# Kernel optimization log

Measured on AMD Instinct MI355X. Metric: run time of the kernel, lower is better.

Reference implementation:

```python
import jax, jax.numpy as jnp
import numpy as np

B, G, T, N = 2, 4, 64, 300
D = 256          # detr_dim == feature_dim
R = 4            # ffn_dim_ratio
MD = 32          # motion_dim


def _xavier(key, shape):
    lim = (6.0 / (shape[0] + shape[1])) ** 0.5
    return jax.random.uniform(key, shape, jnp.float32, -lim, lim)


def setup_inputs() -> dict:
    key = jax.random.key(0)
    ks = jax.random.split(key, 16)
    feats = jax.random.normal(ks[0], (B, G, T, N, D), jnp.float32)
    boxes = jax.random.uniform(ks[1], (B, G, T, N, 4), jnp.float32)
    masks = jax.random.bernoulli(ks[2], 0.3, (B, G, T, N))
    # per-trajectory permutation of frame ids 0..T-1 (unique -> unambiguous scatter)
    u = jax.random.uniform(ks[3], (B, G, N, T))
    times = jnp.swapaxes(jnp.argsort(u, axis=-1).astype(jnp.int32), 2, 3)  # [B,G,T,N]
    return {
        'trajectory_features': feats,
        'trajectory_boxes': boxes,
        'trajectory_masks': masks,
        'trajectory_times': times,
        'adp_w1': _xavier(ks[4], (D, D * R)), 'adp_b1': jnp.zeros((D * R,), jnp.float32),
        'adp_w2': _xavier(ks[5], (D * R, D)), 'adp_b2': jnp.zeros((D,), jnp.float32),
        'norm_g': jnp.ones((D,), jnp.float32), 'norm_b': jnp.zeros((D,), jnp.float32),
        'mot_w1': _xavier(ks[6], (12, MD // 2)), 'mot_b1': jnp.zeros((MD // 2,), jnp.float32),
        'mot_w2': _xavier(ks[7], (MD // 2, MD)), 'mot_b2': jnp.zeros((MD,), jnp.float32),
        'fus_w1': _xavier(ks[8], (D + MD, D)), 'fus_b1': jnp.zeros((D,), jnp.float32),
        'fus_w2': _xavier(ks[9], (D, D)), 'fus_b2': jnp.zeros((D,), jnp.float32),
        'ffn_w1': _xavier(ks[10], (D, D * R)), 'ffn_b1': jnp.zeros((D * R,), jnp.float32),
        'ffn_w2': _xavier(ks[11], (D * R, D)), 'ffn_b2': jnp.zeros((D,), jnp.float32),
        'fnorm_g': jnp.ones((D,), jnp.float32), 'fnorm_b': jnp.zeros((D,), jnp.float32),
    }


def _ffn(x, w1, b1, w2, b2):
    return jax.nn.gelu(x @ w1 + b1, approximate=False) @ w2 + b2


def _ln(x, g, b):
    m = x.mean(-1, keepdims=True)
    v = ((x - m) ** 2).mean(-1, keepdims=True)
    return (x - m) / jnp.sqrt(v + 1e-5) * g + b


def _motion_features(boxes, masks, times, mot_w1, mot_b1, mot_w2, mot_b2):
    # boxes [B,G,T,N,4] -> trajectory-major [B,G,N,T,*]
    b_, g_, t_, n_ = masks.shape
    md = mot_b2.shape[0]
    bx = jnp.swapaxes(boxes, 2, 3)              # [B,G,N,T,4]
    valid = ~jnp.swapaxes(masks, 2, 3)          # [B,G,N,T]
    tm = jnp.swapaxes(times, 2, 3)              # [B,G,N,T]
    # sort valid entries first, by time (stable)
    order = jnp.argsort(jnp.where(valid, tm, t_ + 1), axis=-1)
    sb = jnp.take_along_axis(bx, order[..., None], axis=3)   # sorted boxes
    st = jnp.take_along_axis(tm, order, axis=-1)             # sorted times
    cnt = valid.sum(-1)                                      # [B,G,N]
    pos = jnp.arange(t_)
    in_count = pos[None, None, None, :] < cnt[..., None]
    dt = jnp.maximum(st - jnp.roll(st, 1, axis=-1), 1).astype(sb.dtype)[..., None]
    mask_v = ((pos >= 1)[None, None, None, :] & in_count)[..., None]
    vel = jnp.where(mask_v, (sb - jnp.roll(sb, 1, axis=3)) / dt, 0.0)
    mask_a = ((pos >= 2)[None, None, None, :] & in_count)[..., None]
    acc = jnp.where(mask_a, (vel - jnp.roll(vel, 1, axis=3)) / dt, 0.0)
    mv = jnp.concatenate([sb, vel, acc], axis=-1)            # [B,G,N,T,12]
    enc = jax.nn.gelu(mv @ mot_w1 + mot_b1, approximate=False) @ mot_w2 + mot_b2
    write = in_count & (cnt >= 2)[..., None] & (st < t_)
    frame = jnp.where(write, st, t_)                         # t_ -> dropped
    bi, gi, ni, ti = jnp.meshgrid(jnp.arange(b_), jnp.arange(g_), jnp.arange(n_),
                                  jnp.arange(t_), indexing='ij')
    out = jnp.zeros((b_, g_, t_, n_, md), sb.dtype)
    return out.at[bi, gi, frame, ni].set(enc, mode='drop')


def reference(trajectory_features, trajectory_boxes, trajectory_masks, trajectory_times,
              adp_w1, adp_b1, adp_w2, adp_b2, norm_g, norm_b,
              mot_w1, mot_b1, mot_w2, mot_b2,
              fus_w1, fus_b1, fus_w2, fus_b2,
              ffn_w1, ffn_b1, ffn_w2, ffn_b2, fnorm_g, fnorm_b):
    x = trajectory_features + _ffn(trajectory_features, adp_w1, adp_b1, adp_w2, adp_b2)
    x = _ln(x, norm_g, norm_b)
    motion = _motion_features(trajectory_boxes, trajectory_masks, trajectory_times,
                              mot_w1, mot_b1, mot_w2, mot_b2)
    cat = jnp.concatenate([x, motion], axis=-1)
    fused = jax.nn.gelu(cat @ fus_w1 + fus_b1, approximate=False) @ fus_w2 + fus_b2
    fused = fused + _ffn(fused, ffn_w1, ffn_b1, ffn_w2, ffn_b2)
    fused = _ln(fused, fnorm_g, fnorm_b)
    return fused, motion
```

## Files before the change

### kernel.cpp

```cpp
#include <hip/hip_runtime.h>

typedef __bf16 bf16x8 __attribute__((ext_vector_type(8)));
typedef __bf16 bf16x4 __attribute__((ext_vector_type(4)));
typedef float f32x4 __attribute__((ext_vector_type(4)));

namespace {

constexpr int T_ = 64;
constexpr int N_ = 300;
constexpr int MD_ = 32;
constexpr int BG_ = 8;
constexpr long MROWS_ = (long)BG_ * T_ * N_;
constexpr long FUSED_N = MROWS_ * 256;
constexpr int MB = 32;

constexpr long PA1 = 0;
constexpr long PA2 = 262144;
constexpr long PF1 = 524288;
constexpr long PF2 = 598016;
constexpr long PN1 = 663552;
constexpr long PN2 = 925696;

__device__ __forceinline__ float gelu_f(float x) {
  const float x2 = x * x;
  const float z2 = x * fmaf(x2, 0.07135481627f, 1.5957691216f);
  const float t = __builtin_amdgcn_rcpf(1.0f + __expf(z2));
  return x * (1.0f - t);
}

__device__ __forceinline__ float gelu_exact(float x) {
  return 0.5f * x * (1.0f + erff(x * 0.7071067811865476f));
}

__global__ void k_zero_flag(int* f) { *f = 0; }

__global__ void k_detect_mask(const unsigned char* __restrict__ m, int nbytes,
                              int* __restrict__ f) {
  int i = blockIdx.x * 256 + threadIdx.x;
  if (i < nbytes && (i & 3) != 0 && m[i] != 0) atomicOr(f, 1);
}

__global__ __launch_bounds__(256)
void k_motion(const float* __restrict__ boxes, const void* __restrict__ masks,
              const int* __restrict__ times,
              const float* __restrict__ mw1, const float* __restrict__ mb1,
              const float* __restrict__ mw2, const float* __restrict__ mb2,
              float* __restrict__ motion, const int* __restrict__ flagp) {
  __shared__ int slot[4][T_];
  __shared__ int sts[4][T_];
  __shared__ float sbx[4][T_][4];
  __shared__ float otile[4][T_][MD_];
  const int tid = threadIdx.x;
  const int w = tid >> 6, l = tid & 63;
  const int traj = blockIdx.x * 4 + w;
  const int bg = traj / N_, n = traj - bg * N_;
  const int isbool = *flagp;
  const long idx = ((long)bg * T_ + l) * N_ + n;
  const bool msk = isbool ? (((const unsigned char*)masks)[idx] != 0)
                          : (((const int*)masks)[idx] != 0);
  const bool valid = !msk;
  const int tm = times[idx];

  slot[w][l] = -1;
  sts[w][l] = 0;
  *(float4*)&sbx[w][l][0] = make_float4(0.f, 0.f, 0.f, 0.f);
  __syncthreads();
  if (valid) slot[w][tm] = l;
  __syncthreads();

  const int ot = slot[w][l];
  const bool vp = ot >= 0;
  const unsigned long long bal = __ballot(vp);
  const int cnt = __builtin_popcountll(bal);
  const int pos = __builtin_popcountll(bal & ((1ull << l) - 1ull));
  if (vp) {
    sts[w][pos] = l;
    const float4 bx = *(const float4*)(boxes + (((long)bg * T_ + ot) * N_ + n) * 4);
    *(float4*)&sbx[w][pos][0] = bx;
  }
  __syncthreads();

  const int stp = sts[w][l];
  const int stm1 = sts[w][(l + 63) & 63];
  const float4 sb = *(const float4*)&sbx[w][l][0];
  const float4 sbm = *(const float4*)&sbx[w][(l + 63) & 63][0];
  const float dt = (float)max(stp - stm1, 1);
  const float inv = 1.0f / dt;
  const bool okv = (l >= 1) && (l < cnt);
  float v0 = okv ? (sb.x - sbm.x) * inv : 0.f;
  float v1 = okv ? (sb.y - sbm.y) * inv : 0.f;
  float v2 = okv ? (sb.z - sbm.z) * inv : 0.f;
  float v3 = okv ? (sb.w - sbm.w) * inv : 0.f;
  const float p0 = __shfl_up(v0, 1, 64);
  const float p1 = __shfl_up(v1, 1, 64);
  const float p2 = __shfl_up(v2, 1, 64);
  const float p3 = __shfl_up(v3, 1, 64);
  const bool oka = (l >= 2) && (l < cnt);
  const float a0 = oka ? (v0 - p0) * inv : 0.f;
  const float a1 = oka ? (v1 - p1) * inv : 0.f;
  const float a2 = oka ? (v2 - p2) * inv : 0.f;
  const float a3 = oka ? (v3 - p3) * inv : 0.f;

  const float mv[12] = {sb.x, sb.y, sb.z, sb.w, v0, v1, v2, v3, a0, a1, a2, a3};
  float e1[16];
#pragma unroll
  for (int i = 0; i < 16; ++i) {
    float a = mb1[i];
#pragma unroll
    for (int c = 0; c < 12; ++c) a = fmaf(mv[c], mw1[c * 16 + i], a);
    e1[i] = gelu_exact(a);
  }
  float enc[32];
#pragma unroll
  for (int o = 0; o < 32; ++o) {
    float a = mb2[o];
#pragma unroll
    for (int i = 0; i < 16; ++i) a = fmaf(e1[i], mw2[i * 32 + o], a);
    enc[o] = a;
  }

#pragma unroll
  for (int c = 0; c < 32; c += 4)
    *(float4*)&otile[w][l][c] = make_float4(0.f, 0.f, 0.f, 0.f);
  __syncthreads();
  if (l < cnt && cnt >= 2) {
#pragma unroll
    for (int c = 0; c < 32; ++c) otile[w][stp][c] = enc[c];
  }
  __syncthreads();

  float* mbase = motion + ((long)bg * T_ * N_ + n) * MD_;
  const float4* srcv = (const float4*)&otile[w][l][0];
  float4* dstv = (float4*)(mbase + (long)l * N_ * MD_);
#pragma unroll
  for (int q = 0; q < 8; ++q) dstv[q] = srcv[q];
}

__global__ void k_pack(const float* __restrict__ W, __bf16* __restrict__ P,
                       int K, int NN) {
  int gid = blockIdx.x * 256 + threadIdx.x;
  int total = (K >> 5) * (NN >> 4) * 64;
  if (gid >= total) return;
  int l = gid & 63, f = gid >> 6;
  int NT = NN >> 4;
  int kb = f / NT, nt = f - kb * NT;
  int krow = kb * 32 + (l >> 4) * 8;
  int col = nt * 16 + (l & 15);
  bf16x8 v;
#pragma unroll
  for (int e = 0; e < 8; ++e) v[e] = (__bf16)W[(long)(krow + e) * NN + col];
  *(bf16x8*)(P + (long)gid * 8) = v;
}

template <int NKB, bool MOT, int NT>
__device__ __forceinline__ void produce_chunk(
    const char* regA, const char* regM, char* hb, const __bf16* pb1,
    const float* b1, int r, int wid, int l, int lr, int lk) {
  const int nt0 = r * 8 + wid * 2;
  f32x4 t[2][2];
#pragma unroll
  for (int n = 0; n < 2; ++n) {
    const float4 bv = *(const float4*)(b1 + (nt0 + n) * 16 + lk * 4);
    t[n][0] = f32x4{bv.x, bv.y, bv.z, bv.w};
    t[n][1] = t[n][0];
  }
  const __bf16* wp0 = pb1 + ((long)nt0 << 9) + (l << 3);
  const __bf16* wp1 = wp0 + (1 << 9);
  bf16x8 wa0 = *(const bf16x8*)(wp0);
  bf16x8 wa1 = *(const bf16x8*)(wp1);
  bf16x8 wb0 = wa0, wb1 = wa1;
  if (NKB > 1) {
    wb0 = *(const bf16x8*)(wp0 + ((long)NT << 9));
    wb1 = *(const bf16x8*)(wp1 + ((long)NT << 9));
  }
#pragma unroll
  for (int kb = 0; kb < NKB; ++kb) {
    const bf16x8 wf0 = (kb & 1) ? wb0 : wa0;
    const bf16x8 wf1 = (kb & 1) ? wb1 : wa1;
    if (kb + 2 < NKB) {
      const bf16x8 v0 = *(const bf16x8*)(wp0 + ((long)((kb + 2) * NT) << 9));
      const bf16x8 v1 = *(const bf16x8*)(wp1 + ((long)((kb + 2) * NT) << 9));
      if (kb & 1) { wb0 = v0; wb1 = v1; } else { wa0 = v0; wa1 = v1; }
    }
    __builtin_amdgcn_s_setprio(1);
#pragma unroll
    for (int rt = 0; rt < 2; ++rt) {
      const int row = rt * 16 + lr;
      bf16x8 xf;
      if (MOT && kb == NKB - 1)
        xf = *(const bf16x8*)(regM + row * 64 + ((lk ^ (row & 3)) << 4));
      else
        xf = *(const bf16x8*)(regA + row * 512 +
                              ((((kb << 2) + lk) ^ (row & 7)) << 4));
      t[0][rt] = __builtin_amdgcn_mfma_f32_16x16x32_bf16(wf0, xf, t[0][rt], 0, 0, 0);
      t[1][rt] = __builtin_amdgcn_mfma_f32_16x16x32_bf16(wf1, xf, t[1][rt], 0, 0, 0);
    }
    __builtin_amdgcn_s_setprio(0);
  }
#pragma unroll
  for (int n = 0; n < 2; ++n)
#pragma unroll
    for (int rt = 0; rt < 2; ++rt) {
      const int row = rt * 16 + lr;
      bf16x4 hv;
#pragma unroll
      for (int e = 0; e < 4; ++e) hv[e] = (__bf16)gelu_f(t[n][rt][e]);
      *(bf16x4*)(hb + row * 256 +
                 ((wid * 64 + n * 32 + lk * 8) ^ ((row & 7) << 4))) = hv;
    }
}

__device__ __forceinline__ void consume_chunk(const char* hb,
                                              const __bf16* pb2, int kbg0,
                                              int l, int lr, int lk, int wn,
                                              f32x4 (&acc)[2][4]) {
  const __bf16* wp = pb2 + ((long)(kbg0 * 16 + wn * 4) << 9) + (l << 3);
  bf16x8 bw0[4], bw1[4];
#pragma unroll
  for (int j = 0; j < 4; ++j) bw0[j] = *(const bf16x8*)(wp + ((long)j << 9));
#pragma unroll
  for (int kbl = 0; kbl < 4; ++kbl) {
    if (kbl < 3) {
#pragma unroll
      for (int j = 0; j < 4; ++j)
        bw1[j] = *(const bf16x8*)(wp + ((long)((kbl + 1) * 16 + j) << 9));
    }
    bf16x8 a[2];
#pragma unroll
    for (int m = 0; m < 2; ++m) {
      const int row = m * 16 + lr;
      a[m] = *(const bf16x8*)(hb + row * 256 +
                              ((kbl * 64 + lk * 16) ^ ((row & 7) << 4)));
    }
    __builtin_amdgcn_s_setprio(1);
#pragma unroll
    for (int j = 0; j < 4; ++j)
#pragma unroll
      for (int m = 0; m < 2; ++m)
        acc[m][j] = __builtin_amdgcn_mfma_f32_16x16x32_bf16(a[m], bw0[j],
                                                            acc[m][j], 0, 0, 0);
    __builtin_amdgcn_s_setprio(0);
#pragma unroll
    for (int j = 0; j < 4; ++j) bw0[j] = bw1[j];
  }
}

__global__ __launch_bounds__(256, 3)
void k_mfma(const float* __restrict__ feats, const float* __restrict__ motion,
            const __bf16* __restrict__ pw,
            const float* __restrict__ ba1, const float* __restrict__ ba2,
            const float* __restrict__ ng, const float* __restrict__ nb,
            const float* __restrict__ bf1, const float* __restrict__ bf2,
            const float* __restrict__ bn1, const float* __restrict__ bn2,
            const float* __restrict__ fg, const float* __restrict__ fb,
            float* __restrict__ out) {
  __shared__ __align__(16) char smem[35840];
  char* regA = smem;
  char* hb0 = smem + 16384;
  char* hb1 = smem + 24576;
  char* regM = smem + 32768;
  float* redp = (float*)(smem + 34816);

  const int tid = threadIdx.x;
  const int l = tid & 63, wid = tid >> 6;
  const int lr = l & 15, lk = l >> 4;
  const int wn = wid;
  const int colb = wn * 64;
  const long rowbase = (long)blockIdx.x * MB;

  const __bf16* pa1 = pw + PA1;
  const __bf16* pa2 = pw + PA2;
  const __bf16* pf1 = pw + PF1;
  const __bf16* pf2 = pw + PF2;
  const __bf16* pn1 = pw + PN1;
  const __bf16* pn2 = pw + PN2;

  auto ln_stats = [&](const f32x4 (&acc)[2][4], float (&mean)[2][4],
                      float (&rstd)[2][4]) {
    float s1[2][4], s2[2][4];
#pragma unroll
    for (int m = 0; m < 2; ++m)
#pragma unroll
      for (int e = 0; e < 4; ++e) { s1[m][e] = 0.f; s2[m][e] = 0.f; }
#pragma unroll
    for (int m = 0; m < 2; ++m)
#pragma unroll
      for (int j = 0; j < 4; ++j)
#pragma unroll
        for (int e = 0; e < 4; ++e) {
          s1[m][e] += acc[m][j][e];
          s2[m][e] += acc[m][j][e] * acc[m][j][e];
        }
#pragma unroll
    for (int o = 1; o < 16; o <<= 1)
#pragma unroll
      for (int m = 0; m < 2; ++m)
#pragma unroll
        for (int e = 0; e < 4; ++e) {
          s1[m][e] += __shfl_xor(s1[m][e], o);
          s2[m][e] += __shfl_xor(s2[m][e], o);
        }
    if (lr == 0) {
#pragma unroll
      for (int m = 0; m < 2; ++m)
#pragma unroll
        for (int e = 0; e < 4; ++e) {
          const int row = m * 16 + lk * 4 + e;
          redp[(row * 4 + wn) * 2 + 0] = s1[m][e];
          redp[(row * 4 + wn) * 2 + 1] = s2[m][e];
        }
    }
    __syncthreads();
#pragma unroll
    for (int m = 0; m < 2; ++m)
#pragma unroll
      for (int e = 0; e < 4; ++e) {
        const int row = m * 16 + lk * 4 + e;
        const float S1 = redp[(row * 4 + 0) * 2] + redp[(row * 4 + 1) * 2] +
                         redp[(row * 4 + 2) * 2] + redp[(row * 4 + 3) * 2];
        const float S2 = redp[(row * 4 + 0) * 2 + 1] + redp[(row * 4 + 1) * 2 + 1] +
                         redp[(row * 4 + 2) * 2 + 1] + redp[(row * 4 + 3) * 2 + 1];
        const float mu = S1 * (1.0f / 256.0f);
        const float var = S2 * (1.0f / 256.0f) - mu * mu;
        mean[m][e] = mu;
        rstd[m][e] = rsqrtf(var + 1e-5f);
      }
  };

  f32x4 acc2[2][4];
#pragma unroll
  for (int j = 0; j < 4; ++j) {
    const int col = colb + j * 16 + lr;
    const float bv = ba2[col];
#pragma unroll
    for (int m = 0; m < 2; ++m)
#pragma unroll
      for (int e = 0; e < 4; ++e) {
        const int row = m * 16 + lk * 4 + e;
        acc2[m][j][e] = bv + feats[(rowbase + row) * 256 + col];
      }
  }
#pragma unroll
  for (int it = 0; it < 4; ++it) {
    const int c = tid + it * 256;
    const int row = c >> 5, cc = c & 31;
    const float* src = feats + (rowbase + row) * 256 + cc * 8;
    bf16x8 v;
#pragma unroll
    for (int e = 0; e < 8; ++e) v[e] = (__bf16)src[e];
    *(bf16x8*)(regA + row * 512 + ((cc ^ (row & 7)) << 4)) = v;
  }
  __syncthreads();

  produce_chunk<8, false, 64>(regA, regM, hb0, pa1, ba1, 0, wid, l, lr, lk);
  __syncthreads();
#pragma unroll 1
  for (int r = 0; r < 8; ++r) {
    if (r < 7)
      produce_chunk<8, false, 64>(regA, regM, ((r + 1) & 1) ? hb1 : hb0, pa1,
                                  ba1, r + 1, wid, l, lr, lk);
    consume_chunk((r & 1) ? hb1 : hb0, pa2, r * 4, l, lr, lk, wn, acc2);
    __syncthreads();
  }

  {
    float mean[2][4], rstd[2][4];
    ln_stats(acc2, mean, rstd);
#pragma unroll
    for (int j = 0; j < 4; ++j) {
      const int col = colb + j * 16 + lr;
      const float gv = ng[col], bv = nb[col];
#pragma unroll
      for (int m = 0; m < 2; ++m)
#pragma unroll
        for (int e = 0; e < 4; ++e) {
          const int row = m * 16 + lk * 4 + e;
          const float v = (acc2[m][j][e] - mean[m][e]) * rstd[m][e] * gv + bv;
          *(__bf16*)(regA + row * 512 + (((col >> 3) ^ (row & 7)) << 4) +
                     ((col & 7) << 1)) = (__bf16)v;
        }
    }
    if (tid < 128) {
      const int row = tid >> 2, cc = tid & 3;
      const float* src = motion + (rowbase + row) * 32 + cc * 8;
      bf16x8 v;
#pragma unroll
      for (int e = 0; e < 8; ++e) v[e] = (__bf16)src[e];
      *(bf16x8*)(regM + row * 64 + ((cc ^ (row & 3)) << 4)) = v;
    }
  }
  __syncthreads();

  {
#pragma unroll
    for (int j = 0; j < 4; ++j) {
      const float bv = bf2[colb + j * 16 + lr];
#pragma unroll
      for (int m = 0; m < 2; ++m) acc2[m][j] = {bv, bv, bv, bv};
    }
    produce_chunk<9, true, 16>(regA, regM, hb0, pf1, bf1, 0, wid, l, lr, lk);
    __syncthreads();
    produce_chunk<9, true, 16>(regA, regM, hb1, pf1, bf1, 1, wid, l, lr, lk);
    consume_chunk(hb0, pf2, 0, l, lr, lk, wn, acc2);
    __syncthreads();
    consume_chunk(hb1, pf2, 4, l, lr, lk, wn, acc2);
    __syncthreads();
#pragma unroll
    for (int j = 0; j < 4; ++j) {
      const int col = colb + j * 16 + lr;
      const float bv = bn2[col];
#pragma unroll
      for (int m = 0; m < 2; ++m)
#pragma unroll
        for (int e = 0; e < 4; ++e) {
          const int row = m * 16 + lk * 4 + e;
          const float fv = acc2[m][j][e];
          *(__bf16*)(regA + row * 512 + (((col >> 3) ^ (row & 7)) << 4) +
                     ((col & 7) << 1)) = (__bf16)fv;
          acc2[m][j][e] = fv + bv;
        }
    }
  }
  __syncthreads();

  produce_chunk<8, false, 64>(regA, regM, hb0, pn1, bn1, 0, wid, l, lr, lk);
  __syncthreads();
#pragma unroll 1
  for (int r = 0; r < 8; ++r) {
    if (r < 7)
      produce_chunk<8, false, 64>(regA, regM, ((r + 1) & 1) ? hb1 : hb0, pn1,
                                  bn1, r + 1, wid, l, lr, lk);
    consume_chunk((r & 1) ? hb1 : hb0, pn2, r * 4, l, lr, lk, wn, acc2);
    __syncthreads();
  }

  {
    float mean[2][4], rstd[2][4];
    ln_stats(acc2, mean, rstd);
#pragma unroll
    for (int j = 0; j < 4; ++j) {
      const int col = colb + j * 16 + lr;
      const float gv = fg[col], bv = fb[col];
#pragma unroll
      for (int m = 0; m < 2; ++m)
#pragma unroll
        for (int e = 0; e < 4; ++e) {
          const int row = m * 16 + lk * 4 + e;
          out[(rowbase + row) * 256 + col] =
              (acc2[m][j][e] - mean[m][e]) * rstd[m][e] * gv + bv;
        }
    }
  }
}

}

extern "C" void kernel_launch(void* const* d_in, const int* in_sizes, int n_in,
                              void* d_out, int out_size, void* d_ws, size_t ws_size,
                              hipStream_t stream) {
  const float* feats = (const float*)d_in[0];
  const float* boxes = (const float*)d_in[1];
  const void*  masks = d_in[2];
  const int*   times = (const int*)d_in[3];
  const float* wa1 = (const float*)d_in[4];
  const float* ba1 = (const float*)d_in[5];
  const float* wa2 = (const float*)d_in[6];
  const float* ba2 = (const float*)d_in[7];
  const float* ng  = (const float*)d_in[8];
  const float* nb  = (const float*)d_in[9];
  const float* mw1 = (const float*)d_in[10];
  const float* mb1 = (const float*)d_in[11];
  const float* mw2 = (const float*)d_in[12];
  const float* mb2 = (const float*)d_in[13];
  const float* wf1 = (const float*)d_in[14];
  const float* bf1 = (const float*)d_in[15];
  const float* wf2 = (const float*)d_in[16];
  const float* bf2 = (const float*)d_in[17];
  const float* wn1 = (const float*)d_in[18];
  const float* bn1 = (const float*)d_in[19];
  const float* wn2 = (const float*)d_in[20];
  const float* bn2 = (const float*)d_in[21];
  const float* fg  = (const float*)d_in[22];
  const float* fb  = (const float*)d_in[23];

  float* out_fused = (float*)d_out;
  float* out_motion = out_fused + FUSED_N;
  int* flag = (int*)d_ws;
  __bf16* pwp = (__bf16*)((char*)d_ws + 256);

  const int mask_elems = in_sizes[2];

  k_zero_flag<<<1, 1, 0, stream>>>(flag);
  k_detect_mask<<<(mask_elems + 255) / 256, 256, 0, stream>>>(
      (const unsigned char*)masks, mask_elems, flag);
  k_motion<<<(BG_ * N_) / 4, 256, 0, stream>>>(boxes, masks, times, mw1, mb1, mw2,
                                               mb2, out_motion, flag);

  auto packn = [&](const float* W, long off, int K, int NN) {
    const int total = (K / 32) * (NN / 16) * 64;
    k_pack<<<(total + 255) / 256, 256, 0, stream>>>(W, pwp + off, K, NN);
  };
  packn(wa1, PA1, 256, 1024);
  packn(wa2, PA2, 1024, 256);
  packn(wf1, PF1, 288, 256);
  packn(wf2, PF2, 256, 256);
  packn(wn1, PN1, 256, 1024);
  packn(wn2, PN2, 1024, 256);

  k_mfma<<<(int)(MROWS_ / MB), 256, 0, stream>>>(
      feats, out_motion, pwp, ba1, ba2, ng, nb, bf1, bf2, bn1, bn2, fg, fb,
      out_fused);
}
```

Baseline: 561.9 us.

## Interleave FFN up-projection and down-projection MFMAs within each pipelined round

Adds a fused_round function that runs the next chunk's first-layer MFMAs, loaded with GELU into the write buffer, in the same instruction stream as the current chunk's second-layer MFMAs from the read buffer. Weight loads for both stages are software-prefetched and interleaved, so memory latency and MFMA issue overlap better than two separate sequential calls. The last chunk is consumed separately after the loop. This raises register pressure (both accumulator sets and prefetched weights stay live at once) under the 3-blocks-per-CU launch bound.

```diff
diff --git a/kernel.cpp b/kernel.cpp
--- a/kernel.cpp
+++ b/kernel.cpp
@@ -245,6 +245,87 @@
   }
 }
 
+__device__ __forceinline__ void fused_round(
+    const char* regA, char* hbw, const char* hbr, const __bf16* pb1,
+    const float* b1, int rprod, const __bf16* pb2, int kbg0, int wid, int l,
+    int lr, int lk, int wn, f32x4 (&acc)[2][4]) {
+  constexpr int NT = 64;
+  const int nt0 = rprod * 8 + wid * 2;
+  f32x4 t[2][2];
+#pragma unroll
+  for (int n = 0; n < 2; ++n) {
+    const float4 bv = *(const float4*)(b1 + (nt0 + n) * 16 + lk * 4);
+    t[n][0] = f32x4{bv.x, bv.y, bv.z, bv.w};
+    t[n][1] = t[n][0];
+  }
+  const __bf16* wp0 = pb1 + ((long)nt0 << 9) + (l << 3);
+  const __bf16* wp1 = wp0 + (1 << 9);
+  bf16x8 wa0 = *(const bf16x8*)(wp0);
+  bf16x8 wa1 = *(const bf16x8*)(wp1);
+  bf16x8 wb0 = *(const bf16x8*)(wp0 + ((long)NT << 9));
+  bf16x8 wb1 = *(const bf16x8*)(wp1 + ((long)NT << 9));
+  const __bf16* wp = pb2 + ((long)(kbg0 * 16 + wn * 4) << 9) + (l << 3);
+  bf16x8 bw0[4], bw1[4];
+#pragma unroll
+  for (int j = 0; j < 4; ++j) bw0[j] = *(const bf16x8*)(wp + ((long)j << 9));
+#pragma unroll
+  for (int kb = 0; kb < 8; ++kb) {
+    const bf16x8 wf0 = (kb & 1) ? wb0 : wa0;
+    const bf16x8 wf1 = (kb & 1) ? wb1 : wa1;
+    if (kb + 2 < 8) {
+      const bf16x8 v0 = *(const bf16x8*)(wp0 + ((long)((kb + 2) * NT) << 9));
+      const bf16x8 v1 = *(const bf16x8*)(wp1 + ((long)((kb + 2) * NT) << 9));
+      if (kb & 1) { wb0 = v0; wb1 = v1; } else { wa0 = v0; wa1 = v1; }
+    }
+    __builtin_amdgcn_s_setprio(1);
+#pragma unroll
+    for (int rt = 0; rt < 2; ++rt) {
+      const int row = rt * 16 + lr;
+      const bf16x8 xf = *(const bf16x8*)(regA + row * 512 +
+                                         ((((kb << 2) + lk) ^ (row & 7)) << 4));
+      t[0][rt] = __builtin_amdgcn_mfma_f32_16x16x32_bf16(wf0, xf, t[0][rt], 0, 0, 0);
+      t[1][rt] = __builtin_amdgcn_mfma_f32_16x16x32_bf16(wf1, xf, t[1][rt], 0, 0, 0);
+    }
+    __builtin_amdgcn_s_setprio(0);
+    if (kb & 1) {
+      const int kbl = kb >> 1;
+      if (kbl < 3) {
+#pragma unroll
+        for (int j = 0; j < 4; ++j)
+          bw1[j] = *(const bf16x8*)(wp + ((long)((kbl + 1) * 16 + j) << 9));
+      }
+      bf16x8 a[2];
+#pragma unroll
+      for (int m = 0; m < 2; ++m) {
+        const int row = m * 16 + lr;
+        a[m] = *(const bf16x8*)(hbr + row * 256 +
+                                ((kbl * 64 + lk * 16) ^ ((row & 7) << 4)));
+      }
+      __builtin_amdgcn_s_setprio(1);
+#pragma unroll
+      for (int j = 0; j < 4; ++j)
+#pragma unroll
+        for (int m = 0; m < 2; ++m)
+          acc[m][j] = __builtin_amdgcn_mfma_f32_16x16x32_bf16(a[m], bw0[j],
+                                                              acc[m][j], 0, 0, 0);
+      __builtin_amdgcn_s_setprio(0);
+#pragma unroll
+      for (int j = 0; j < 4; ++j) bw0[j] = bw1[j];
+    }
+  }
+#pragma unroll
+  for (int n = 0; n < 2; ++n)
+#pragma unroll
+    for (int rt = 0; rt < 2; ++rt) {
+      const int row = rt * 16 + lr;
+      bf16x4 hv;
+#pragma unroll
+      for (int e = 0; e < 4; ++e) hv[e] = (__bf16)gelu_f(t[n][rt][e]);
+      *(bf16x4*)(hbw + row * 256 +
+                 ((wid * 64 + n * 32 + lk * 8) ^ ((row & 7) << 4))) = hv;
+    }
+}
+
 __global__ __launch_bounds__(256, 3)
 void k_mfma(const float* __restrict__ feats, const float* __restrict__ motion,
             const __bf16* __restrict__ pw,
@@ -355,13 +436,13 @@
   produce_chunk<8, false, 64>(regA, regM, hb0, pa1, ba1, 0, wid, l, lr, lk);
   __syncthreads();
 #pragma unroll 1
-  for (int r = 0; r < 8; ++r) {
-    if (r < 7)
-      produce_chunk<8, false, 64>(regA, regM, ((r + 1) & 1) ? hb1 : hb0, pa1,
-                                  ba1, r + 1, wid, l, lr, lk);
-    consume_chunk((r & 1) ? hb1 : hb0, pa2, r * 4, l, lr, lk, wn, acc2);
+  for (int r = 0; r < 7; ++r) {
+    fused_round(regA, ((r + 1) & 1) ? hb1 : hb0, (r & 1) ? hb1 : hb0, pa1, ba1,
+                r + 1, pa2, r * 4, wid, l, lr, lk, wn, acc2);
     __syncthreads();
   }
+  consume_chunk(hb1, pa2, 28, l, lr, lk, wn, acc2);
+  __syncthreads();
 
   {
     float mean[2][4], rstd[2][4];
@@ -426,13 +507,13 @@
   produce_chunk<8, false, 64>(regA, regM, hb0, pn1, bn1, 0, wid, l, lr, lk);
   __syncthreads();
 #pragma unroll 1
-  for (int r = 0; r < 8; ++r) {
-    if (r < 7)
-      produce_chunk<8, false, 64>(regA, regM, ((r + 1) & 1) ? hb1 : hb0, pn1,
-                                  bn1, r + 1, wid, l, lr, lk);
-    consume_chunk((r & 1) ? hb1 : hb0, pn2, r * 4, l, lr, lk, wn, acc2);
+  for (int r = 0; r < 7; ++r) {
+    fused_round(regA, ((r + 1) & 1) ? hb1 : hb0, (r & 1) ? hb1 : hb0, pn1, bn1,
+                r + 1, pn2, r * 4, wid, l, lr, lk, wn, acc2);
     __syncthreads();
   }
+  consume_chunk(hb1, pn2, 28, l, lr, lk, wn, acc2);
+  __syncthreads();
 
   {
     float mean[2][4], rstd[2][4];
```

New measurement: 569.0 us. No clear change (+1.3%).
